# Kernel tuning notes

Measured on AMD Instinct MI355X. Metric: run time of the kernel, lower is better.

## Reference

```python
import jax, jax.numpy as jnp
import numpy as np

B_SZ, SEQ, D_IN, D_ST, D_OUT = 16, 8192, 128, 128, 128


def setup_inputs() -> dict:
    key = jax.random.key(0)
    ku, ka, kb, kc, kd = jax.random.split(key, 5)
    u = jax.random.normal(ku, (B_SZ, SEQ, D_IN), dtype=jnp.float32)
    # A scaled to spectral radius ~0.9 so the long recurrence stays stable
    A = jax.random.normal(ka, (D_ST, D_ST), dtype=jnp.float32) * (0.9 / np.sqrt(D_ST))
    B = jax.random.normal(kb, (D_ST, D_IN), dtype=jnp.float32) * (1.0 / np.sqrt(D_IN))
    C = jax.random.normal(kc, (D_OUT, D_ST), dtype=jnp.float32) * (1.0 / np.sqrt(D_ST))
    D = jax.random.normal(kd, (D_OUT, D_IN), dtype=jnp.float32) * (1.0 / np.sqrt(D_IN))
    return {"u": u, "A": A, "B": B, "C": C, "D": D}


def reference(u, A, B, C, D):
    # x_t = x_{t-1} A^T + u_t B^T ; y_t = x_t C^T + u_t D^T ; x_0 = 0
    batch = u.shape[0]
    state0 = jnp.zeros((batch, A.shape[0]), dtype=u.dtype)

    def step(state, u_t):  # state: [B, S_dim], u_t: [B, D_in]
        new_state = state @ A.T + u_t @ B.T
        y = new_state @ C.T + u_t @ D.T
        return new_state, y

    u_t_first = jnp.swapaxes(u, 0, 1)  # [SEQ, B, D_in]
    _, ys = jax.lax.scan(step, state0, u_t_first)
    return jnp.swapaxes(ys, 0, 1)  # [B, SEQ, D_out]
```

## Files before the change

kernel.cpp:

```cpp
#include <hip/hip_runtime.h>


#define SEQ 8192
#define DD  128
#define WIN 12

typedef __bf16 bf16t;
typedef __bf16 bf16x8 __attribute__((ext_vector_type(8)));
typedef float  f32x4  __attribute__((ext_vector_type(4)));

#define MFMA(a,b,c) __builtin_amdgcn_mfma_f32_16x16x32_bf16(a,b,c,0,0,0)

__device__ __forceinline__ int swc(int r, int c) {
    int g = c >> 3;
    g = (g & ~7) | ((g ^ r) & 7);
    return (g << 3) | (c & 7);
}
__device__ __forceinline__ bf16x8 lds_frag(const bf16t* T, int stride, int row, int col) {
    return *(const bf16x8*)(T + row * stride + swc(row, col));
}
__device__ __forceinline__ bf16x8 cvt8(float4 a, float4 b) {
    bf16x8 r;
    r[0]=(bf16t)a.x; r[1]=(bf16t)a.y; r[2]=(bf16t)a.z; r[3]=(bf16t)a.w;
    r[4]=(bf16t)b.x; r[5]=(bf16t)b.y; r[6]=(bf16t)b.z; r[7]=(bf16t)b.w;
    return r;
}
__device__ __forceinline__ bf16x8 bzero8() {
    bf16x8 z;
#pragma unroll
    for (int e = 0; e < 8; e++) z[e] = (bf16t)0.f;
    return z;
}
__device__ __forceinline__ f32x4 fzero4() { f32x4 z = {0.f, 0.f, 0.f, 0.f}; return z; }

__global__ __launch_bounds__(512, 2) void k_squares(const float* __restrict__ A,
                                                    float* __restrict__ Sq,
                                                    float* __restrict__ Iden,
                                                    bf16t* __restrict__ E1pad) {
    int tid = threadIdx.x, lane = tid & 63, wid = tid >> 6;
    if (blockIdx.x == 1) {
        for (int i = tid; i < 16384; i += 512)
            Iden[i] = ((i >> 7) == (i & 127)) ? 1.f : 0.f;
        bf16x8 z = bzero8();
        for (int i = tid; i < WIN * 16 * 128 / 8; i += 512)
            *(bf16x8*)(E1pad + i * 8) = z;
        return;
    }
    __shared__ bf16t H0[128*128], T0[128*128], H1[128*128], T1[128*128];
    {
        int r = tid >> 2, c0 = (tid & 3) * 32;
#pragma unroll
        for (int e = 0; e < 4; e++) {
            float4 va = *(const float4*)(A + r*128 + c0 + e*8);
            float4 vb = *(const float4*)(A + r*128 + c0 + e*8 + 4);
            bf16x8 h = cvt8(va, vb);
            *(bf16x8*)(H0 + r*128 + swc(r, c0 + e*8)) = h;
#pragma unroll
            for (int x = 0; x < 8; x++) {
                int cc = c0 + e*8 + x;
                T0[cc*128 + swc(cc, r)] = h[x];
            }
        }
    }
    __syncthreads();
    bf16t *cH = H0, *cT = T0, *nH = H1, *nT = T1;
    for (int lvl = 0; lvl < 6; lvl++) {
        f32x4 acc[8];
#pragma unroll
        for (int nf = 0; nf < 8; nf++) acc[nf] = fzero4();
        int m = 16*wid + (lane & 15);
#pragma unroll
        for (int q = 0; q < 4; q++) {
            bf16x8 af = lds_frag(cH, 128, m, q*32 + ((lane >> 4) << 3));
#pragma unroll
            for (int nf = 0; nf < 8; nf++) {
                bf16x8 bv = lds_frag(cT, 128, nf*16 + (lane & 15), q*32 + ((lane >> 4) << 3));
                acc[nf] = MFMA(af, bv, acc[nf]);
            }
        }
#pragma unroll
        for (int nf = 0; nf < 8; nf++)
#pragma unroll
            for (int rr = 0; rr < 4; rr++) {
                int row = 16*wid + ((lane >> 4) << 2) + rr;
                int col = nf*16 + (lane & 15);
                float v = acc[nf][rr];
                bf16t hv = (bf16t)v;
                nH[row*128 + swc(row, col)] = hv;
                nT[col*128 + swc(col, row)] = hv;
                Sq[lvl*16384 + row*128 + col] = v;
            }
        __syncthreads();
        bf16t* t;
        t = cH; cH = nH; nH = t;
        t = cT; cT = nT; nT = t;
    }
}

__global__ __launch_bounds__(512) void k_mats(const float* __restrict__ A,
                                              const float* __restrict__ B,
                                              const float* __restrict__ C,
                                              const float* __restrict__ Dm,
                                              const float* __restrict__ Sq,
                                              const float* __restrict__ Iden,
                                              bf16t* __restrict__ KbigT,
                                              bf16t* __restrict__ DistT,
                                              bf16t* __restrict__ WdT,
                                              bf16t* __restrict__ QT) {
    __shared__ bf16t Hc[128*128], Hn[128*128], Tg[128*128];
    int tid = threadIdx.x, lane = tid & 63, wid = tid >> 6;
    int bid = blockIdx.x;
    const float* G[10] = {A, B, C, Sq, Sq + 16384, Sq + 2*16384,
                          Sq + 3*16384, Sq + 4*16384, Sq + 5*16384, Iden};
    int ch[6]; int nc = 0;
    bf16t* dst = nullptr; long dstride = 128;
    bool plusD = false;
    if (bid < 8) {
        int d = bid;
        if (d & 4) ch[nc++] = 4;
        if (d & 2) ch[nc++] = 3;
        if (d & 1) ch[nc++] = 0;
        ch[nc++] = 1;
        if (nc == 1) ch[nc++] = 9;
        dst = KbigT + (7 - d) * 128; dstride = 1024;
    } else if (bid < 20) {
        int e = bid - 8;
        if (e & 8) ch[nc++] = 8;
        if (e & 4) ch[nc++] = 7;
        if (e & 2) ch[nc++] = 6;
        if (e & 1) ch[nc++] = 5;
        if (nc == 0) ch[nc++] = 9;
        if (nc == 1) ch[nc++] = 9;
        dst = DistT + e * 16384;
    } else if (bid < 28) {
        int d = bid - 20;
        ch[nc++] = 2;
        if (d & 4) ch[nc++] = 4;
        if (d & 2) ch[nc++] = 3;
        if (d & 1) ch[nc++] = 0;
        ch[nc++] = 1;
        plusD = (d == 0);
        dst = WdT + d * 16384;
    } else {
        int k = bid - 28 + 1;
        ch[nc++] = 2;
        if (k & 8) ch[nc++] = 5;
        if (k & 4) ch[nc++] = 4;
        if (k & 2) ch[nc++] = 3;
        if (k & 1) ch[nc++] = 0;
        dst = QT + (k - 1) * 16384;
    }
    {
        const float* g0 = G[ch[0]];
        int r = tid >> 2, c0 = (tid & 3) * 32;
#pragma unroll
        for (int e = 0; e < 4; e++) {
            float4 va = *(const float4*)(g0 + r*128 + c0 + e*8);
            float4 vb = *(const float4*)(g0 + r*128 + c0 + e*8 + 4);
            *(bf16x8*)(Hc + r*128 + swc(r, c0 + e*8)) = cvt8(va, vb);
        }
    }
    f32x4 acc[8];
    bf16t* cur = Hc; bf16t* nxt = Hn;
    for (int i = 1; i < nc; i++) {
        const float* g = G[ch[i]];
        __syncthreads();
        {
            int r = tid >> 2, c0 = (tid & 3) * 32;
#pragma unroll
            for (int e = 0; e < 4; e++) {
                float4 va = *(const float4*)(g + r*128 + c0 + e*8);
                float4 vb = *(const float4*)(g + r*128 + c0 + e*8 + 4);
                bf16x8 h = cvt8(va, vb);
#pragma unroll
                for (int x = 0; x < 8; x++) {
                    int cc = c0 + e*8 + x;
                    Tg[cc*128 + swc(cc, r)] = h[x];
                }
            }
        }
        __syncthreads();
#pragma unroll
        for (int nf = 0; nf < 8; nf++) acc[nf] = fzero4();
        int m = 16*wid + (lane & 15);
#pragma unroll
        for (int q = 0; q < 4; q++) {
            bf16x8 af = lds_frag(cur, 128, m, q*32 + ((lane >> 4) << 3));
#pragma unroll
            for (int nf = 0; nf < 8; nf++) {
                bf16x8 bv = lds_frag(Tg, 128, nf*16 + (lane & 15), q*32 + ((lane >> 4) << 3));
                acc[nf] = MFMA(af, bv, acc[nf]);
            }
        }
        if (i + 1 < nc) {
#pragma unroll
            for (int nf = 0; nf < 8; nf++)
#pragma unroll
                for (int rr = 0; rr < 4; rr++) {
                    int row = 16*wid + ((lane >> 4) << 2) + rr;
                    int col = nf*16 + (lane & 15);
                    nxt[row*128 + swc(row, col)] = (bf16t)acc[nf][rr];
                }
            bf16t* t = cur; cur = nxt; nxt = t;
        }
    }
#pragma unroll
    for (int nf = 0; nf < 8; nf++)
#pragma unroll
        for (int rr = 0; rr < 4; rr++) {
            int row = 16*wid + ((lane >> 4) << 2) + rr;
            int col = nf*16 + (lane & 15);
            float v = acc[nf][rr];
            if (plusD) v += Dm[row*128 + col];
            dst[(long)row * dstride + col] = (bf16t)v;
        }
}

__global__ __launch_bounds__(512, 2) void k_pass1(const float* __restrict__ u,
                                                  const bf16t* __restrict__ KbigT,
                                                  bf16t* __restrict__ E1pad) {
    __shared__ bf16t U[64*1024];
    int tid = threadIdx.x, lane = tid & 63, w = tid >> 6;
    int c0 = blockIdx.x * 4;
    int n = (w << 4) + (lane & 15), kg = lane >> 4;
    bf16x8 bc[32];
#pragma unroll
    for (int s = 0; s < 32; s++)
        bc[s] = *(const bf16x8*)(KbigT + n*1024 + s*32 + kg*8);
    {
        int row = tid >> 3, cl = row >> 4, b = row & 15, cb = (tid & 7) * 128;
        const float* up = u + (long)b*SEQ*DD + (long)(c0 + cl)*1024 + cb;
#pragma unroll
        for (int e = 0; e < 16; e++) {
            float4 v0 = *(const float4*)(up + e*8);
            float4 v1 = *(const float4*)(up + e*8 + 4);
            *(bf16x8*)(U + row*1024 + swc(row, cb + e*8)) = cvt8(v0, v1);
        }
    }
    __syncthreads();
    f32x4 acc[4][2];
#pragma unroll
    for (int m = 0; m < 4; m++) { acc[m][0] = fzero4(); acc[m][1] = fzero4(); }
#pragma unroll
    for (int s = 0; s < 32; s++) {
#pragma unroll
        for (int m = 0; m < 4; m++) {
            bf16x8 af = lds_frag(U, 1024, m*16 + (lane & 15), s*32 + kg*8);
            acc[m][s & 1] = MFMA(af, bc[s], acc[m][s & 1]);
        }
    }
#pragma unroll
    for (int m = 0; m < 4; m++) {
        f32x4 a = acc[m][0] + acc[m][1];
#pragma unroll
        for (int rr = 0; rr < 4; rr++) {
            int b = (kg << 2) + rr;
            E1pad[((long)(WIN + c0 + m)*16 + b)*128 + n] = (bf16t)a[rr];
        }
    }
}

__global__ __launch_bounds__(512, 2) void k_passE(const bf16t* __restrict__ E1pad,
                                                  const bf16t* __restrict__ DistT,
                                                  bf16t* __restrict__ Xent) {
    __shared__ bf16t Et[256*128];
    int tid = threadIdx.x, lane = tid & 63, w = tid >> 6;
    int c0 = blockIdx.x * 4;
    int n = (w << 4) + (lane & 15), kg = lane >> 4;
    {
        const bf16t* src = E1pad + (long)c0*16*128;
        int row = tid >> 1, cb = (tid & 1) * 64;
#pragma unroll
        for (int e = 0; e < 8; e++) {
            bf16x8 v = *(const bf16x8*)(src + row*128 + cb + e*8);
            *(bf16x8*)(Et + row*128 + swc(row, cb + e*8)) = v;
        }
    }
    __syncthreads();
    f32x4 acc[4][2];
#pragma unroll
    for (int m = 0; m < 4; m++) { acc[m][0] = fzero4(); acc[m][1] = fzero4(); }
#pragma unroll
    for (int j = 1; j <= WIN; j++) {
#pragma unroll
        for (int kk = 0; kk < 4; kk++) {
            bf16x8 bf = *(const bf16x8*)(DistT + (long)(j-1)*16384 + n*128 + kk*32 + kg*8);
#pragma unroll
            for (int m = 0; m < 4; m++) {
                bf16x8 af = lds_frag(Et, 128, (m + WIN - j)*16 + (lane & 15), kk*32 + kg*8);
                acc[m][j & 1] = MFMA(af, bf, acc[m][j & 1]);
            }
        }
    }
#pragma unroll
    for (int m = 0; m < 4; m++) {
        f32x4 a = acc[m][0] + acc[m][1];
#pragma unroll
        for (int rr = 0; rr < 4; rr++) {
            int b = (kg << 2) + rr;
            Xent[((long)(c0 + m)*16 + b)*128 + n] = (bf16t)a[rr];
        }
    }
}

__global__ __launch_bounds__(512, 2) void k_pass2(const float* __restrict__ u,
                                                  const bf16t* __restrict__ Xent,
                                                  const bf16t* __restrict__ WdT,
                                                  const bf16t* __restrict__ QT,
                                                  float* __restrict__ out) {
    __shared__ bf16t U[64*1024];
    __shared__ bf16t X[64*128];
    int tid = threadIdx.x, lane = tid & 63, w = tid >> 6;
    int c0 = blockIdx.x * 4;
    int n = (w << 4) + (lane & 15), kg = lane >> 4;
    bf16x8 bc[4][4];
#pragma unroll
    for (int d = 0; d < 4; d++)
#pragma unroll
        for (int k4 = 0; k4 < 4; k4++)
            bc[d][k4] = *(const bf16x8*)(WdT + (long)d*16384 + n*128 + k4*32 + kg*8);
    {
        int row = tid >> 3, cl = row >> 4, b = row & 15, cb = (tid & 7) * 128;
        const float* up = u + (long)b*SEQ*DD + (long)(c0 + cl)*1024 + cb;
#pragma unroll
        for (int e = 0; e < 16; e++) {
            float4 v0 = *(const float4*)(up + e*8);
            float4 v1 = *(const float4*)(up + e*8 + 4);
            *(bf16x8*)(U + row*1024 + swc(row, cb + e*8)) = cvt8(v0, v1);
        }
    }
    {
        const bf16t* xs = Xent + (long)c0*16*128;
        int row = tid >> 3, cb = (tid & 7) * 16;
#pragma unroll
        for (int e = 0; e < 2; e++) {
            bf16x8 v = *(const bf16x8*)(xs + row*128 + cb + e*8);
            *(bf16x8*)(X + row*128 + swc(row, cb + e*8)) = v;
        }
    }
    __syncthreads();
    f32x4 acc[4][8];
#pragma unroll
    for (int m = 0; m < 4; m++)
#pragma unroll
        for (int t = 0; t < 8; t++) acc[m][t] = fzero4();
#pragma unroll
    for (int p = 0; p < 8; p++) {
#pragma unroll
        for (int k4 = 0; k4 < 4; k4++) {
            int s = p*4 + k4;
            bf16x8 af[4];
#pragma unroll
            for (int m = 0; m < 4; m++)
                af[m] = lds_frag(U, 1024, m*16 + (lane & 15), s*32 + kg*8);
#pragma unroll
            for (int t = p; t < 8; t++) {
                int d = t - p;
                bf16x8 bf = (d < 4) ? bc[d][k4]
                    : *(const bf16x8*)(WdT + (long)d*16384 + n*128 + k4*32 + kg*8);
#pragma unroll
                for (int m = 0; m < 4; m++) acc[m][t] = MFMA(af[m], bf, acc[m][t]);
            }
        }
    }
#pragma unroll
    for (int k4 = 0; k4 < 4; k4++) {
        bf16x8 af[4];
#pragma unroll
        for (int m = 0; m < 4; m++)
            af[m] = lds_frag(X, 128, m*16 + (lane & 15), k4*32 + kg*8);
#pragma unroll
        for (int t = 0; t < 8; t++) {
            bf16x8 bf = *(const bf16x8*)(QT + (long)t*16384 + n*128 + k4*32 + kg*8);
#pragma unroll
            for (int m = 0; m < 4; m++) acc[m][t] = MFMA(af[m], bf, acc[m][t]);
        }
    }
#pragma unroll
    for (int m = 0; m < 4; m++)
#pragma unroll
        for (int t = 0; t < 8; t++)
#pragma unroll
            for (int rr = 0; rr < 4; rr++) {
                int b = (kg << 2) + rr;
                out[(long)b*SEQ*DD + ((long)(c0 + m)*8 + t)*DD + n] = acc[m][t][rr];
            }
}

extern "C" void kernel_launch(void* const* d_in, const int* in_sizes, int n_in,
                              void* d_out, int out_size, void* d_ws, size_t ws_size,
                              hipStream_t stream) {
    (void)in_sizes; (void)n_in; (void)out_size; (void)ws_size;
    const float* u = (const float*)d_in[0];
    const float* A = (const float*)d_in[1];
    const float* B = (const float*)d_in[2];
    const float* C = (const float*)d_in[3];
    const float* D = (const float*)d_in[4];
    float* out = (float*)d_out;
    float* Sq    = (float*)d_ws;
    float* Iden  = Sq + 6*16384;
    bf16t* KbigT = (bf16t*)(Iden + 16384);
    bf16t* DistT = KbigT + 131072;
    bf16t* WdT   = DistT + 12*16384;
    bf16t* QT    = WdT + 8*16384;
    bf16t* E1pad = QT + 8*16384;
    bf16t* Xent  = E1pad + (long)(WIN + 1024)*2048;

    k_squares<<<2,  512, 0, stream>>>(A, Sq, Iden, E1pad);
    k_mats  <<<36,  512, 0, stream>>>(A, B, C, D, Sq, Iden, KbigT, DistT, WdT, QT);
    k_pass1 <<<256, 512, 0, stream>>>(u, KbigT, E1pad);
    k_passE <<<256, 512, 0, stream>>>(E1pad, DistT, Xent);
    k_pass2 <<<256, 512, 0, stream>>>(u, Xent, WdT, QT, out);
}
```

Measured before the change: 124.5 us.

## Halve chunks per block, double grid, and widen truncation window to 16

Each pass kernel now handles 2 chunks per block instead of 4, so the grids grow from 256 to 512 blocks to fill more CUs on the MI355X. The block-to-block carry window WIN rises from 12 to 16, which means more distance matrices are built and more passE MFMAs run per block. pass1 drops the register-resident B fragments in favour of per-step global loads, and the u staging is reorganised so consecutive threads read consecutive memory. The aim is better occupancy and lower register pressure, at the cost of more redundant halo loads and extra window work per block.

```diff
diff --git a/kernel.cpp b/kernel.cpp
--- a/kernel.cpp
+++ b/kernel.cpp
@@ -3,7 +3,7 @@
 
 #define SEQ 8192
 #define DD  128
-#define WIN 12
+#define WIN 16
 
 typedef __bf16 bf16t;
 typedef __bf16 bf16x8 __attribute__((ext_vector_type(8)));
@@ -123,7 +123,7 @@
         ch[nc++] = 1;
         if (nc == 1) ch[nc++] = 9;
         dst = KbigT + (7 - d) * 128; dstride = 1024;
-    } else if (bid < 20) {
+    } else if (bid < 24) {
         int e = bid - 8;
         if (e & 8) ch[nc++] = 8;
         if (e & 4) ch[nc++] = 7;
@@ -132,8 +132,8 @@
         if (nc == 0) ch[nc++] = 9;
         if (nc == 1) ch[nc++] = 9;
         dst = DistT + e * 16384;
-    } else if (bid < 28) {
-        int d = bid - 20;
+    } else if (bid < 32) {
+        int d = bid - 24;
         ch[nc++] = 2;
         if (d & 4) ch[nc++] = 4;
         if (d & 2) ch[nc++] = 3;
@@ -142,7 +142,7 @@
         plusD = (d == 0);
         dst = WdT + d * 16384;
     } else {
-        int k = bid - 28 + 1;
+        int k = bid - 32 + 1;
         ch[nc++] = 2;
         if (k & 8) ch[nc++] = 5;
         if (k & 4) ch[nc++] = 4;
@@ -216,41 +216,43 @@
         }
 }
 
+__device__ __forceinline__ void stage_u2(const float* __restrict__ u, int c0,
+                                         bf16t* __restrict__ U, int tid) {
+    int row = tid >> 4;
+    int cl = row >> 4, b = row & 15;
+    const float* up = u + (long)b * SEQ * DD + (long)(c0 + cl) * 1024 + (tid & 15) * 8;
+#pragma unroll
+    for (int e = 0; e < 8; e++) {
+        int col = (tid & 15) * 8 + e * 128;
+        float4 v0 = *(const float4*)(up + e * 128);
+        float4 v1 = *(const float4*)(up + e * 128 + 4);
+        *(bf16x8*)(U + row * 1024 + swc(row, col)) = cvt8(v0, v1);
+    }
+}
+
 __global__ __launch_bounds__(512, 2) void k_pass1(const float* __restrict__ u,
                                                   const bf16t* __restrict__ KbigT,
                                                   bf16t* __restrict__ E1pad) {
-    __shared__ bf16t U[64*1024];
+    __shared__ bf16t U[32*1024];
     int tid = threadIdx.x, lane = tid & 63, w = tid >> 6;
-    int c0 = blockIdx.x * 4;
+    int c0 = blockIdx.x * 2;
     int n = (w << 4) + (lane & 15), kg = lane >> 4;
-    bf16x8 bc[32];
-#pragma unroll
-    for (int s = 0; s < 32; s++)
-        bc[s] = *(const bf16x8*)(KbigT + n*1024 + s*32 + kg*8);
-    {
-        int row = tid >> 3, cl = row >> 4, b = row & 15, cb = (tid & 7) * 128;
-        const float* up = u + (long)b*SEQ*DD + (long)(c0 + cl)*1024 + cb;
-#pragma unroll
-        for (int e = 0; e < 16; e++) {
-            float4 v0 = *(const float4*)(up + e*8);
-            float4 v1 = *(const float4*)(up + e*8 + 4);
-            *(bf16x8*)(U + row*1024 + swc(row, cb + e*8)) = cvt8(v0, v1);
-        }
-    }
+    stage_u2(u, c0, U, tid);
     __syncthreads();
-    f32x4 acc[4][2];
-#pragma unroll
-    for (int m = 0; m < 4; m++) { acc[m][0] = fzero4(); acc[m][1] = fzero4(); }
+    f32x4 acc[2][2];
+#pragma unroll
+    for (int m = 0; m < 2; m++) { acc[m][0] = fzero4(); acc[m][1] = fzero4(); }
 #pragma unroll
     for (int s = 0; s < 32; s++) {
-#pragma unroll
-        for (int m = 0; m < 4; m++) {
+        bf16x8 bk = *(const bf16x8*)(KbigT + n*1024 + s*32 + kg*8);
+#pragma unroll
+        for (int m = 0; m < 2; m++) {
             bf16x8 af = lds_frag(U, 1024, m*16 + (lane & 15), s*32 + kg*8);
-            acc[m][s & 1] = MFMA(af, bc[s], acc[m][s & 1]);
-        }
-    }
-#pragma unroll
-    for (int m = 0; m < 4; m++) {
+            acc[m][s & 1] = MFMA(af, bk, acc[m][s & 1]);
+        }
+    }
+#pragma unroll
+    for (int m = 0; m < 2; m++) {
         f32x4 a = acc[m][0] + acc[m][1];
 #pragma unroll
         for (int rr = 0; rr < 4; rr++) {
@@ -263,37 +265,36 @@
 __global__ __launch_bounds__(512, 2) void k_passE(const bf16t* __restrict__ E1pad,
                                                   const bf16t* __restrict__ DistT,
                                                   bf16t* __restrict__ Xent) {
-    __shared__ bf16t Et[256*128];
+    __shared__ bf16t Et[272*128];
     int tid = threadIdx.x, lane = tid & 63, w = tid >> 6;
-    int c0 = blockIdx.x * 4;
+    int c0 = blockIdx.x * 2;
     int n = (w << 4) + (lane & 15), kg = lane >> 4;
     {
         const bf16t* src = E1pad + (long)c0*16*128;
-        int row = tid >> 1, cb = (tid & 1) * 64;
-#pragma unroll
-        for (int e = 0; e < 8; e++) {
-            bf16x8 v = *(const bf16x8*)(src + row*128 + cb + e*8);
-            *(bf16x8*)(Et + row*128 + swc(row, cb + e*8)) = v;
+        for (int idx = tid; idx < 272*16; idx += 512) {
+            int row = idx >> 4, gc = (idx & 15) * 8;
+            bf16x8 v = *(const bf16x8*)(src + row*128 + gc);
+            *(bf16x8*)(Et + row*128 + swc(row, gc)) = v;
         }
     }
     __syncthreads();
-    f32x4 acc[4][2];
-#pragma unroll
-    for (int m = 0; m < 4; m++) { acc[m][0] = fzero4(); acc[m][1] = fzero4(); }
+    f32x4 acc[2][2];
+#pragma unroll
+    for (int m = 0; m < 2; m++) { acc[m][0] = fzero4(); acc[m][1] = fzero4(); }
 #pragma unroll
     for (int j = 1; j <= WIN; j++) {
 #pragma unroll
         for (int kk = 0; kk < 4; kk++) {
             bf16x8 bf = *(const bf16x8*)(DistT + (long)(j-1)*16384 + n*128 + kk*32 + kg*8);
 #pragma unroll
-            for (int m = 0; m < 4; m++) {
+            for (int m = 0; m < 2; m++) {
                 bf16x8 af = lds_frag(Et, 128, (m + WIN - j)*16 + (lane & 15), kk*32 + kg*8);
                 acc[m][j & 1] = MFMA(af, bf, acc[m][j & 1]);
             }
         }
     }
 #pragma unroll
-    for (int m = 0; m < 4; m++) {
+    for (int m = 0; m < 2; m++) {
         f32x4 a = acc[m][0] + acc[m][1];
 #pragma unroll
         for (int rr = 0; rr < 4; rr++) {
@@ -308,40 +309,28 @@
                                                   const bf16t* __restrict__ WdT,
                                                   const bf16t* __restrict__ QT,
                                                   float* __restrict__ out) {
-    __shared__ bf16t U[64*1024];
-    __shared__ bf16t X[64*128];
+    __shared__ bf16t U[32*1024];
+    __shared__ bf16t X[32*128];
     int tid = threadIdx.x, lane = tid & 63, w = tid >> 6;
-    int c0 = blockIdx.x * 4;
+    int c0 = blockIdx.x * 2;
     int n = (w << 4) + (lane & 15), kg = lane >> 4;
-    bf16x8 bc[4][4];
-#pragma unroll
-    for (int d = 0; d < 4; d++)
+    bf16x8 bc[2][4];
+#pragma unroll
+    for (int d = 0; d < 2; d++)
 #pragma unroll
         for (int k4 = 0; k4 < 4; k4++)
             bc[d][k4] = *(const bf16x8*)(WdT + (long)d*16384 + n*128 + k4*32 + kg*8);
-    {
-        int row = tid >> 3, cl = row >> 4, b = row & 15, cb = (tid & 7) * 128;
-        const float* up = u + (long)b*SEQ*DD + (long)(c0 + cl)*1024 + cb;
-#pragma unroll
-        for (int e = 0; e < 16; e++) {
-            float4 v0 = *(const float4*)(up + e*8);
-            float4 v1 = *(const float4*)(up + e*8 + 4);
-            *(bf16x8*)(U + row*1024 + swc(row, cb + e*8)) = cvt8(v0, v1);
-        }
-    }
+    stage_u2(u, c0, U, tid);
     {
         const bf16t* xs = Xent + (long)c0*16*128;
-        int row = tid >> 3, cb = (tid & 7) * 16;
-#pragma unroll
-        for (int e = 0; e < 2; e++) {
-            bf16x8 v = *(const bf16x8*)(xs + row*128 + cb + e*8);
-            *(bf16x8*)(X + row*128 + swc(row, cb + e*8)) = v;
-        }
+        int row = tid >> 4, gc = (tid & 15) * 8;
+        bf16x8 v = *(const bf16x8*)(xs + row*128 + gc);
+        *(bf16x8*)(X + row*128 + swc(row, gc)) = v;
     }
     __syncthreads();
-    f32x4 acc[4][8];
-#pragma unroll
-    for (int m = 0; m < 4; m++)
+    f32x4 acc[2][8];
+#pragma unroll
+    for (int m = 0; m < 2; m++)
 #pragma unroll
         for (int t = 0; t < 8; t++) acc[m][t] = fzero4();
 #pragma unroll
@@ -349,35 +338,31 @@
 #pragma unroll
         for (int k4 = 0; k4 < 4; k4++) {
             int s = p*4 + k4;
-            bf16x8 af[4];
-#pragma unroll
-            for (int m = 0; m < 4; m++)
-                af[m] = lds_frag(U, 1024, m*16 + (lane & 15), s*32 + kg*8);
+            bf16x8 af0 = lds_frag(U, 1024, (lane & 15),      s*32 + kg*8);
+            bf16x8 af1 = lds_frag(U, 1024, 16 + (lane & 15), s*32 + kg*8);
 #pragma unroll
             for (int t = p; t < 8; t++) {
                 int d = t - p;
-                bf16x8 bf = (d < 4) ? bc[d][k4]
+                bf16x8 bf = (d < 2) ? bc[d][k4]
                     : *(const bf16x8*)(WdT + (long)d*16384 + n*128 + k4*32 + kg*8);
-#pragma unroll
-                for (int m = 0; m < 4; m++) acc[m][t] = MFMA(af[m], bf, acc[m][t]);
+                acc[0][t] = MFMA(af0, bf, acc[0][t]);
+                acc[1][t] = MFMA(af1, bf, acc[1][t]);
             }
         }
     }
 #pragma unroll
     for (int k4 = 0; k4 < 4; k4++) {
-        bf16x8 af[4];
-#pragma unroll
-        for (int m = 0; m < 4; m++)
-            af[m] = lds_frag(X, 128, m*16 + (lane & 15), k4*32 + kg*8);
+        bf16x8 af0 = lds_frag(X, 128, (lane & 15),      k4*32 + kg*8);
+        bf16x8 af1 = lds_frag(X, 128, 16 + (lane & 15), k4*32 + kg*8);
 #pragma unroll
         for (int t = 0; t < 8; t++) {
             bf16x8 bf = *(const bf16x8*)(QT + (long)t*16384 + n*128 + k4*32 + kg*8);
-#pragma unroll
-            for (int m = 0; m < 4; m++) acc[m][t] = MFMA(af[m], bf, acc[m][t]);
-        }
-    }
-#pragma unroll
-    for (int m = 0; m < 4; m++)
+            acc[0][t] = MFMA(af0, bf, acc[0][t]);
+            acc[1][t] = MFMA(af1, bf, acc[1][t]);
+        }
+    }
+#pragma unroll
+    for (int m = 0; m < 2; m++)
 #pragma unroll
         for (int t = 0; t < 8; t++)
 #pragma unroll
@@ -401,14 +386,14 @@
     float* Iden  = Sq + 6*16384;
     bf16t* KbigT = (bf16t*)(Iden + 16384);
     bf16t* DistT = KbigT + 131072;
-    bf16t* WdT   = DistT + 12*16384;
+    bf16t* WdT   = DistT + 16*16384;
     bf16t* QT    = WdT + 8*16384;
     bf16t* E1pad = QT + 8*16384;
     bf16t* Xent  = E1pad + (long)(WIN + 1024)*2048;
 
     k_squares<<<2,  512, 0, stream>>>(A, Sq, Iden, E1pad);
-    k_mats  <<<36,  512, 0, stream>>>(A, B, C, D, Sq, Iden, KbigT, DistT, WdT, QT);
-    k_pass1 <<<256, 512, 0, stream>>>(u, KbigT, E1pad);
-    k_passE <<<256, 512, 0, stream>>>(E1pad, DistT, Xent);
-    k_pass2 <<<256, 512, 0, stream>>>(u, Xent, WdT, QT, out);
-}
+    k_mats  <<<40,  512, 0, stream>>>(A, B, C, D, Sq, Iden, KbigT, DistT, WdT, QT);
+    k_pass1 <<<512, 512, 0, stream>>>(u, KbigT, E1pad);
+    k_passE <<<512, 512, 0, stream>>>(E1pad, DistT, Xent);
+    k_pass2 <<<512, 512, 0, stream>>>(u, Xent, WdT, QT, out);
+}
```

After: 144.7 us. +16.3%, slower.
